# Optimization experiments

Hardware: AMD Instinct MI355X
Metric: run time of the kernel (lower is better)

Reference implementation:

```python
import jax, jax.numpy as jnp
import numpy as np
from jax import lax

EPSILON = float(np.finfo(np.float32).tiny)
K = 8
TAU = 1.0
HARD = False
B, N = 4096, 8192


def setup_inputs() -> dict:
    key = jax.random.key(0)
    k1, k2 = jax.random.split(key)
    scores = jax.random.normal(k1, (B, N), dtype=jnp.float32)
    # Gumbel(0,1) noise, precomputed for determinism: g = -log(-log(U))
    u = jax.random.uniform(k2, (B, N), dtype=jnp.float32, minval=1e-10, maxval=1.0)
    g = -jnp.log(-jnp.log(u))
    return {"scores": scores, "g": g}


def reference(scores, g):
    s = scores + g  # perturbed logits [B, N]
    khot = jnp.zeros_like(s)
    onehot = jnp.zeros_like(s)

    def step(carry, _):
        s, khot, onehot = carry
        khot_mask = jnp.maximum(1.0 - onehot, EPSILON)
        s = s + jnp.log(khot_mask)
        onehot = jax.nn.softmax(s / TAU, axis=1)
        khot = khot + onehot
        return (s, khot, onehot), None

    (s, khot, onehot), _ = lax.scan(step, (s, khot, onehot), None, length=K)

    if HARD:
        _, ind = lax.top_k(khot, K)  # [B, K]
        khot_hard = jnp.zeros_like(khot).at[jnp.arange(B)[:, None], ind].set(1.0)
        return khot_hard - lax.stop_gradient(khot) + khot
    return khot
```

## Files before the change

### kernel.cpp

```cpp
#include <hip/hip_runtime.h>
#include <math.h>


#define BROWS 4096
#define NCOLS 8192
#define KITER 8
#define THREADS 256
#define VECS 8
#define NWAVES (THREADS / 64)
#define M0 24.0f

typedef float f32x4 __attribute__((ext_vector_type(4)));
typedef float f32x2 __attribute__((ext_vector_type(2)));

__global__ __launch_bounds__(THREADS)
void subset_op_kernel(const float* __restrict__ scores,
                      const float* __restrict__ g,
                      float* __restrict__ out) {
  const int tid = threadIdx.x;
  const int lane = tid & 63;
  const int wave = tid >> 6;
  const long long rbase = (long long)blockIdx.x * NCOLS;

  f32x2 w2[2 * VECS], kh2[2 * VECS];

  float sum = 0.0f;
#pragma unroll
  for (int j = 0; j < VECS; ++j) {
    const int off = j * 1024 + tid * 4;
    const f32x4 sv = *(const f32x4*)(scores + rbase + off);
    const f32x4 gv = *(const f32x4*)(g + rbase + off);
    f32x2 lo, hi;
    lo.x = __expf(sv.x + gv.x - M0);
    lo.y = __expf(sv.y + gv.y - M0);
    hi.x = __expf(sv.z + gv.z - M0);
    hi.y = __expf(sv.w + gv.w - M0);
    w2[2 * j] = lo; w2[2 * j + 1] = hi;
    kh2[2 * j] = (f32x2){0.0f, 0.0f};
    kh2[2 * j + 1] = (f32x2){0.0f, 0.0f};
    sum += (lo.x + lo.y) + (hi.x + hi.y);
  }

  __shared__ float red[2][NWAVES];

#pragma unroll 1
  for (int k = 0; k < KITER; ++k) {
    float ps = sum;
#pragma unroll
    for (int off = 32; off > 0; off >>= 1) ps += __shfl_xor(ps, off);
    if (lane == 0) red[k & 1][wave] = ps;
    __syncthreads();
    const f32x4 rv = *(const f32x4*)red[k & 1];
    const float tot = (rv.x + rv.y) + (rv.z + rv.w);
    const float inv = __builtin_amdgcn_rcpf(tot);
    const f32x2 iv = {inv, inv};

    f32x2 s0 = {0.0f, 0.0f}, s1 = {0.0f, 0.0f};
    f32x2 s2 = {0.0f, 0.0f}, s3 = {0.0f, 0.0f};
#pragma unroll
    for (int j = 0; j < 2 * VECS; ++j) {
      const f32x2 oh = w2[j] * iv;
      kh2[j] += oh;
      w2[j] = __builtin_elementwise_fma(-oh, w2[j], w2[j]);
      if ((j & 3) == 0)      s0 += w2[j];
      else if ((j & 3) == 1) s1 += w2[j];
      else if ((j & 3) == 2) s2 += w2[j];
      else                   s3 += w2[j];
    }
    const f32x2 sv2 = (s0 + s1) + (s2 + s3);
    sum = sv2.x + sv2.y;
  }

#pragma unroll
  for (int j = 0; j < VECS; ++j) {
    const int off = j * 1024 + tid * 4;
    f32x4 v;
    v.x = kh2[2 * j].x;     v.y = kh2[2 * j].y;
    v.z = kh2[2 * j + 1].x; v.w = kh2[2 * j + 1].y;
    __builtin_nontemporal_store(v, (f32x4*)(out + rbase + off));
  }
}

extern "C" void kernel_launch(void* const* d_in, const int* in_sizes, int n_in,
                              void* d_out, int out_size, void* d_ws, size_t ws_size,
                              hipStream_t stream) {
  const float* scores = (const float*)d_in[0];
  const float* g = (const float*)d_in[1];
  float* out = (float*)d_out;
  (void)in_sizes; (void)n_in; (void)out_size; (void)d_ws; (void)ws_size;

  subset_op_kernel<<<BROWS, THREADS, 0, stream>>>(scores, g, out);
}
```

Baseline: 69.08 us.

## Process multiple rows per block with register prefetch of next row

Each block now handles eight consecutive rows and loads the next row's scores and noise into registers while the current row's eight softmax iterations run. The aim is to hide global-load latency behind compute and to amortise block launch overhead. In exchange the grid shrinks eightfold and register pressure grows, which lowers the number of waves in flight and the memory-level parallelism available.

```diff
diff --git a/kernel.cpp b/kernel.cpp
--- a/kernel.cpp
+++ b/kernel.cpp
@@ -6,6 +6,8 @@
 #define NCOLS 8192
 #define KITER 8
 #define THREADS 256
+#define RPB 8
+#define GRID (BROWS / RPB)
 #define VECS 8
 #define NWAVES (THREADS / 64)
 #define M0 24.0f
@@ -20,64 +22,88 @@
   const int tid = threadIdx.x;
   const int lane = tid & 63;
   const int wave = tid >> 6;
-  const long long rbase = (long long)blockIdx.x * NCOLS;
-
-  f32x2 w2[2 * VECS], kh2[2 * VECS];
-
-  float sum = 0.0f;
-#pragma unroll
-  for (int j = 0; j < VECS; ++j) {
-    const int off = j * 1024 + tid * 4;
-    const f32x4 sv = *(const f32x4*)(scores + rbase + off);
-    const f32x4 gv = *(const f32x4*)(g + rbase + off);
-    f32x2 lo, hi;
-    lo.x = __expf(sv.x + gv.x - M0);
-    lo.y = __expf(sv.y + gv.y - M0);
-    hi.x = __expf(sv.z + gv.z - M0);
-    hi.y = __expf(sv.w + gv.w - M0);
-    w2[2 * j] = lo; w2[2 * j + 1] = hi;
-    kh2[2 * j] = (f32x2){0.0f, 0.0f};
-    kh2[2 * j + 1] = (f32x2){0.0f, 0.0f};
-    sum += (lo.x + lo.y) + (hi.x + hi.y);
-  }
+  const long long row0 = (long long)blockIdx.x * RPB;
 
   __shared__ float red[2][NWAVES];
 
-#pragma unroll 1
-  for (int k = 0; k < KITER; ++k) {
-    float ps = sum;
+  f32x4 ss[VECS], sg[VECS];
+  {
+    const float* sp = scores + row0 * NCOLS;
+    const float* gp = g + row0 * NCOLS;
 #pragma unroll
-    for (int off = 32; off > 0; off >>= 1) ps += __shfl_xor(ps, off);
-    if (lane == 0) red[k & 1][wave] = ps;
-    __syncthreads();
-    const f32x4 rv = *(const f32x4*)red[k & 1];
-    const float tot = (rv.x + rv.y) + (rv.z + rv.w);
-    const float inv = __builtin_amdgcn_rcpf(tot);
-    const f32x2 iv = {inv, inv};
-
-    f32x2 s0 = {0.0f, 0.0f}, s1 = {0.0f, 0.0f};
-    f32x2 s2 = {0.0f, 0.0f}, s3 = {0.0f, 0.0f};
-#pragma unroll
-    for (int j = 0; j < 2 * VECS; ++j) {
-      const f32x2 oh = w2[j] * iv;
-      kh2[j] += oh;
-      w2[j] = __builtin_elementwise_fma(-oh, w2[j], w2[j]);
-      if ((j & 3) == 0)      s0 += w2[j];
-      else if ((j & 3) == 1) s1 += w2[j];
-      else if ((j & 3) == 2) s2 += w2[j];
-      else                   s3 += w2[j];
+    for (int j = 0; j < VECS; ++j) {
+      const int off = j * 1024 + tid * 4;
+      ss[j] = *(const f32x4*)(sp + off);
+      sg[j] = *(const f32x4*)(gp + off);
     }
-    const f32x2 sv2 = (s0 + s1) + (s2 + s3);
-    sum = sv2.x + sv2.y;
   }
 
+#pragma unroll 1
+  for (int r = 0; r < RPB; ++r) {
+    f32x2 w2[2 * VECS], kh2[2 * VECS];
+    float sum = 0.0f;
 #pragma unroll
-  for (int j = 0; j < VECS; ++j) {
-    const int off = j * 1024 + tid * 4;
-    f32x4 v;
-    v.x = kh2[2 * j].x;     v.y = kh2[2 * j].y;
-    v.z = kh2[2 * j + 1].x; v.w = kh2[2 * j + 1].y;
-    __builtin_nontemporal_store(v, (f32x4*)(out + rbase + off));
+    for (int j = 0; j < VECS; ++j) {
+      const f32x4 t = ss[j] + sg[j];
+      f32x2 lo, hi;
+      lo.x = __expf(t.x - M0); lo.y = __expf(t.y - M0);
+      hi.x = __expf(t.z - M0); hi.y = __expf(t.w - M0);
+      w2[2 * j] = lo; w2[2 * j + 1] = hi;
+      kh2[2 * j] = (f32x2){0.0f, 0.0f};
+      kh2[2 * j + 1] = (f32x2){0.0f, 0.0f};
+      sum += (lo.x + lo.y) + (hi.x + hi.y);
+    }
+
+    if (r + 1 < RPB) {
+      const float* sp = scores + (row0 + r + 1) * NCOLS;
+      const float* gp = g + (row0 + r + 1) * NCOLS;
+#pragma unroll
+      for (int j = 0; j < VECS; ++j) {
+        const int off = j * 1024 + tid * 4;
+        ss[j] = *(const f32x4*)(sp + off);
+        sg[j] = *(const f32x4*)(gp + off);
+      }
+    }
+
+#pragma unroll 1
+    for (int k = 0; k < KITER; ++k) {
+      float ps = sum;
+#pragma unroll
+      for (int off = 32; off > 0; off >>= 1) ps += __shfl_xor(ps, off);
+      if (lane == 0) red[k & 1][wave] = ps;
+      __syncthreads();
+      const f32x4 rv = *(const f32x4*)red[k & 1];
+      const float tot = (rv.x + rv.y) + (rv.z + rv.w);
+      const float inv = __builtin_amdgcn_rcpf(tot);
+      const f32x2 iv = {inv, inv};
+
+      f32x2 s0 = {0.0f, 0.0f}, s1 = {0.0f, 0.0f};
+      f32x2 s2 = {0.0f, 0.0f}, s3 = {0.0f, 0.0f};
+#pragma unroll
+      for (int j = 0; j < 2 * VECS; ++j) {
+        const f32x2 oh = w2[j] * iv;
+        kh2[j] += oh;
+        w2[j] = __builtin_elementwise_fma(-oh, w2[j], w2[j]);
+        if ((j & 3) == 0)      s0 += w2[j];
+        else if ((j & 3) == 1) s1 += w2[j];
+        else if ((j & 3) == 2) s2 += w2[j];
+        else                   s3 += w2[j];
+      }
+      const f32x2 sv2 = (s0 + s1) + (s2 + s3);
+      sum = sv2.x + sv2.y;
+    }
+
+    {
+      float* op = out + (row0 + r) * NCOLS;
+#pragma unroll
+      for (int j = 0; j < VECS; ++j) {
+        const int off = j * 1024 + tid * 4;
+        f32x4 v;
+        v.x = kh2[2 * j].x;     v.y = kh2[2 * j].y;
+        v.z = kh2[2 * j + 1].x; v.w = kh2[2 * j + 1].y;
+        __builtin_nontemporal_store(v, (f32x4*)(op + off));
+      }
+    }
   }
 }
 
@@ -89,5 +115,5 @@
   float* out = (float*)d_out;
   (void)in_sizes; (void)n_in; (void)out_size; (void)d_ws; (void)ws_size;
 
-  subset_op_kernel<<<BROWS, THREADS, 0, stream>>>(scores, g, out);
+  subset_op_kernel<<<GRID, THREADS, 0, stream>>>(scores, g, out);
 }
```

New measurement: 74.96 us. 1.09x slower.
